# Optimization experiments

Measured on AMD Instinct MI355X. Metric: run time of the kernel, lower is better.

## Reference

```python
import jax, jax.numpy as jnp
import numpy as np

D_MODEL = 1024
N_HEADS = 16
D_HEAD = D_MODEL // N_HEADS
ROPE_THETA = 10000.0


def apply_rope(x, positions):
    # x: [b, h, s, d], positions: [s]
    half = x.shape[-1] // 2
    inv_freq = ROPE_THETA ** (-jnp.arange(half, dtype=x.dtype) * 2.0 / x.shape[-1])
    ang = positions.astype(x.dtype)[:, None] * inv_freq[None, :]  # [s, half]
    cos, sin = jnp.cos(ang), jnp.sin(ang)
    x1, x2 = x[..., 0::2], x[..., 1::2]  # rotate interleaved pairs (x_{2k}, x_{2k+1})
    out_even = x1 * cos - x2 * sin
    out_odd = x1 * sin + x2 * cos
    return jnp.stack([out_even, out_odd], axis=-1).reshape(x.shape)


def setup_inputs() -> dict:
    key = jax.random.key(0)
    k1, k2, k3 = jax.random.split(key, 3)
    b, s = 4, 2048
    x = jax.random.normal(k1, (b, s, D_MODEL), dtype=jnp.float32)
    w_qkv = jax.random.normal(k2, (3 * D_MODEL, D_MODEL), dtype=jnp.float32) * (D_MODEL ** -0.5)
    w_out = jax.random.normal(k3, (D_MODEL, D_MODEL), dtype=jnp.float32) * (D_MODEL ** -0.5)
    return {"x": x, "w_qkv": w_qkv, "w_out": w_out}


def reference(x, w_qkv, w_out):
    b, s, _ = x.shape
    qkv = jnp.einsum('bsd,ed->bse', x, w_qkv)  # fused QKV projection
    qkv = qkv.reshape(b, s, 3, N_HEADS, D_HEAD).transpose(2, 0, 3, 1, 4)  # [3, b, h, s, d]
    q, k, v = qkv[0], qkv[1], qkv[2]
    positions = jnp.arange(s)
    q = apply_rope(q, positions)
    k = apply_rope(k, positions)
    scale = 1.0 / np.sqrt(D_HEAD)
    scores = jnp.einsum('bhqd,bhkd->bhqk', q, k) * scale
    causal = jnp.tril(jnp.ones((s, s), dtype=bool))
    scores = jnp.where(causal, scores, jnp.finfo(scores.dtype).min)
    attn = jax.nn.softmax(scores, axis=-1)
    out = jnp.einsum('bhqk,bhkd->bhqd', attn, v)
    out = out.transpose(0, 2, 1, 3).reshape(b, s, D_MODEL)  # b h s d -> b s (h d)
    return jnp.einsum('bsd,ed->bse', out, w_out)
```

## Files before the change

### kernel.cpp

```cpp
#include <hip/hip_runtime.h>
#include <math.h>

#define D_MODEL 1024
#define NH      16
#define DH      64
#define S_LEN   2048
#define BATCH   4

typedef unsigned short u16;
typedef __attribute__((ext_vector_type(8))) short s8v;
typedef __attribute__((ext_vector_type(4))) float f4v;

#define MFMA(a, b, c) __builtin_amdgcn_mfma_f32_16x16x32_bf16((a), (b), (c), 0, 0, 0)

__device__ inline u16 f2bf(float f) {
  unsigned u = __float_as_uint(f);
  u += 0x7fffu + ((u >> 16) & 1u);
  return (u16)(u >> 16);
}
__device__ inline float bf2f(u16 h) {
  return __uint_as_float(((unsigned)h) << 16);
}
__device__ inline u16 f2bf_trunc(float f) {
  return (u16)(__float_as_uint(f) >> 16);
}
__device__ inline void split4(const float4 v, short4& h4, short4& l4) {
  u16 hx = f2bf(v.x), hy = f2bf(v.y), hz = f2bf(v.z), hw = f2bf(v.w);
  h4 = make_short4((short)hx, (short)hy, (short)hz, (short)hw);
  l4 = make_short4((short)f2bf_trunc(v.x - bf2f(hx)), (short)f2bf_trunc(v.y - bf2f(hy)),
                   (short)f2bf_trunc(v.z - bf2f(hz)), (short)f2bf_trunc(v.w - bf2f(hw)));
}

__global__ void rope_table_kernel(float* __restrict__ tab) {
  int i = blockIdx.x * 256 + threadIdx.x;
  if (i >= S_LEN * 32) return;
  int s = i >> 5;
  int p = i & 31;
  float invf = (float)pow(10000.0, -(double)p / 32.0);
  float ang = (float)s * invf;
  tab[i]         = cosf(ang);
  tab[65536 + i] = sinf(ang);
}

template <int MODE>
__global__ __launch_bounds__(256) void gemm_mfma(
    const float* __restrict__ A, const float* __restrict__ B,
    float* __restrict__ C,
    u16* __restrict__ qh, u16* __restrict__ ql,
    u16* __restrict__ kh, u16* __restrict__ kl,
    float* __restrict__ vw,
    const float* __restrict__ tab,
    int M, int N, int K)
{
  __shared__ short As[2][128][40];
  __shared__ short Bs[2][128][40];

  const int tid  = threadIdx.x;
  const int lane = tid & 63;
  const int wave = tid >> 6;
  const int wm = wave >> 1, wn = wave & 1;
  const int m0 = blockIdx.y * 128;
  const int n0 = blockIdx.x * 128;

  const int lr = lane & 15;
  const int lk = (lane >> 4) * 8;

  f4v acc[4][4] = {};

  float4 av[4], bv[4];
#pragma unroll
  for (int q = 0; q < 4; ++q) {
    int f = q * 256 + tid;
    int r = f >> 3, kk = (f & 7) * 4;
    av[q] = *(const float4*)&A[(size_t)(m0 + r) * K + kk];
    bv[q] = *(const float4*)&B[(size_t)(n0 + r) * K + kk];
  }

  for (int k0 = 0; k0 < K; k0 += 32) {
    __syncthreads();
#pragma unroll
    for (int q = 0; q < 4; ++q) {
      int f = q * 256 + tid;
      int r = f >> 3, kk = (f & 7) * 4;
      short4 h4, l4;
      split4(av[q], h4, l4);
      *(short4*)&As[0][r][kk] = h4;  *(short4*)&As[1][r][kk] = l4;
      split4(bv[q], h4, l4);
      *(short4*)&Bs[0][r][kk] = h4;  *(short4*)&Bs[1][r][kk] = l4;
    }
    __syncthreads();

    if (k0 + 32 < K) {
#pragma unroll
      for (int q = 0; q < 4; ++q) {
        int f = q * 256 + tid;
        int r = f >> 3, kk = (f & 7) * 4;
        av[q] = *(const float4*)&A[(size_t)(m0 + r) * K + k0 + 32 + kk];
        bv[q] = *(const float4*)&B[(size_t)(n0 + r) * K + k0 + 32 + kk];
      }
    }

    s8v ah[4], al[4], bh[4], bl[4];
#pragma unroll
    for (int x = 0; x < 4; ++x) {
      ah[x] = *(const s8v*)&As[0][wm * 64 + x * 16 + lr][lk];
      al[x] = *(const s8v*)&As[1][wm * 64 + x * 16 + lr][lk];
      bh[x] = *(const s8v*)&Bs[0][wn * 64 + x * 16 + lr][lk];
      bl[x] = *(const s8v*)&Bs[1][wn * 64 + x * 16 + lr][lk];
    }
#pragma unroll
    for (int mf = 0; mf < 4; ++mf)
#pragma unroll
      for (int nf = 0; nf < 4; ++nf) {
        acc[mf][nf] = MFMA(ah[mf], bh[nf], acc[mf][nf]);
        acc[mf][nf] = MFMA(al[mf], bh[nf], acc[mf][nf]);
        acc[mf][nf] = MFMA(ah[mf], bl[nf], acc[mf][nf]);
      }
  }

  if (MODE == 0) {
#pragma unroll
    for (int mf = 0; mf < 4; ++mf)
#pragma unroll
      for (int nf = 0; nf < 4; ++nf) {
        int c = n0 + wn * 64 + nf * 16 + lr;
#pragma unroll
        for (int i = 0; i < 4; ++i) {
          int m = m0 + wm * 64 + mf * 16 + (lane >> 4) * 4 + i;
          C[(size_t)m * N + c] = acc[mf][nf][i];
        }
      }
  } else {
#pragma unroll
    for (int nf = 0; nf < 4; ++nf) {
      int c = n0 + wn * 64 + nf * 16 + lr;
      int t = c >> 10;
      int h = (c & 1023) >> 6;
      int d = c & 63;
#pragma unroll
      for (int mf = 0; mf < 4; ++mf)
#pragma unroll
        for (int i = 0; i < 4; ++i) {
          int m = m0 + wm * 64 + mf * 16 + (lane >> 4) * 4 + i;
          int b = m >> 11, s = m & 2047;
          float v  = acc[mf][nf][i];
          float pv = __shfl_xor(v, 1);
          size_t off = ((size_t)(b * NH + h) * S_LEN + s) * DH + d;
          if (t == 2) {
            vw[off] = v;
          } else {
            int p = d >> 1;
            float co = tab[s * 32 + p], si = tab[65536 + s * 32 + p];
            float res = ((d & 1) == 0) ? (v * co - pv * si)
                                       : (pv * si + v * co);
            u16 hi = f2bf(res);
            u16 lo = f2bf_trunc(res - bf2f(hi));
            ((t == 0) ? qh : kh)[off] = hi;
            ((t == 0) ? ql : kl)[off] = lo;
          }
        }
    }
  }
}

__global__ __launch_bounds__(256) void vtrans_kernel(
    const float* __restrict__ vw, u16* __restrict__ vth, u16* __restrict__ vtl)
{
  __shared__ float T[64][65];
  const int tid = threadIdx.x;
  const int st = blockIdx.x, bh = blockIdx.y;
  const int s0 = st * 64;
#pragma unroll
  for (int it = 0; it < 4; ++it) {
    int f = it * 256 + tid;
    int r = f >> 4, c4 = (f & 15) * 4;
    float4 v = *(const float4*)&vw[((size_t)bh * S_LEN + s0 + r) * DH + c4];
    T[r][c4 + 0] = v.x; T[r][c4 + 1] = v.y; T[r][c4 + 2] = v.z; T[r][c4 + 3] = v.w;
  }
  __syncthreads();
#pragma unroll
  for (int it = 0; it < 16; ++it) {
    int f = it * 256 + tid;
    int d = f >> 6, sc = f & 63;
    float v = T[sc][d];
    u16 hi = f2bf(v);
    size_t off = ((size_t)bh * DH + d) * S_LEN + s0 + sc;
    vth[off] = hi;
    vtl[off] = f2bf_trunc(v - bf2f(hi));
  }
}

__global__ __launch_bounds__(256) void attn3_kernel(
    const u16* __restrict__ qhp, const u16* __restrict__ qlp,
    const u16* __restrict__ khp, const u16* __restrict__ klp,
    const u16* __restrict__ vthp, const u16* __restrict__ vtlp,
    float* __restrict__ ow)
{
  __shared__ u16 Kh[64][72], Kl[64][72];
  __shared__ u16 Vh[64][72], Vl[64][72];
  __shared__ u16 Ph[4][16][72], Pl[4][16][72];

  const int tid  = threadIdx.x;
  const int lane = tid & 63;
  const int w    = tid >> 6;
  const int bid = blockIdx.x;
  const int swz = (bid & 7) * 256 + (bid >> 3);
  const int bh  = swz >> 5;
  const int qt  = 31 - (swz & 31);
  const int q0  = qt * 64;

  const int lr = lane & 15;
  const int lk = (lane >> 4) * 8;
  const int rg = (lane >> 4) * 4;

  const size_t kvbase = (size_t)bh * S_LEN * DH;
  const size_t vtbase = (size_t)bh * DH * S_LEN;

  const int sr  = tid >> 2;
  const int sc0 = (tid & 3) * 16;

  const u16* qrow_h = qhp + kvbase + (size_t)(q0 + w * 16 + lr) * DH;
  const u16* qrow_l = qlp + kvbase + (size_t)(q0 + w * 16 + lr) * DH;
  s8v qfh[2], qfl[2];
#pragma unroll
  for (int c = 0; c < 2; ++c) {
    qfh[c] = *(const s8v*)(qrow_h + c * 32 + lk);
    qfl[c] = *(const s8v*)(qrow_l + c * 32 + lk);
  }

  float m_run[4] = {-3.0e38f, -3.0e38f, -3.0e38f, -3.0e38f};
  float l_run[4] = {0.f, 0.f, 0.f, 0.f};
  f4v o[4] = {};

  s8v rkh[2], rkl[2], rvh[2], rvl[2];
  {
    const size_t koff = kvbase + (size_t)sr * DH + sc0;
    const size_t voff = vtbase + (size_t)sr * S_LEN + 0 + sc0;
    rkh[0] = *(const s8v*)(khp + koff);   rkh[1] = *(const s8v*)(khp + koff + 8);
    rkl[0] = *(const s8v*)(klp + koff);   rkl[1] = *(const s8v*)(klp + koff + 8);
    rvh[0] = *(const s8v*)(vthp + voff);  rvh[1] = *(const s8v*)(vthp + voff + 8);
    rvl[0] = *(const s8v*)(vtlp + voff);  rvl[1] = *(const s8v*)(vtlp + voff + 8);
  }

  for (int kt = 0; kt <= qt; ++kt) {
    __syncthreads();
    *(s8v*)&Kh[sr][sc0] = rkh[0];  *(s8v*)&Kh[sr][sc0 + 8] = rkh[1];
    *(s8v*)&Kl[sr][sc0] = rkl[0];  *(s8v*)&Kl[sr][sc0 + 8] = rkl[1];
    *(s8v*)&Vh[sr][sc0] = rvh[0];  *(s8v*)&Vh[sr][sc0 + 8] = rvh[1];
    *(s8v*)&Vl[sr][sc0] = rvl[0];  *(s8v*)&Vl[sr][sc0 + 8] = rvl[1];
    __syncthreads();

    if (kt < qt) {
      const int kn = (kt + 1) * 64;
      const size_t koff = kvbase + (size_t)(kn + sr) * DH + sc0;
      const size_t voff = vtbase + (size_t)sr * S_LEN + kn + sc0;
      rkh[0] = *(const s8v*)(khp + koff);   rkh[1] = *(const s8v*)(khp + koff + 8);
      rkl[0] = *(const s8v*)(klp + koff);   rkl[1] = *(const s8v*)(klp + koff + 8);
      rvh[0] = *(const s8v*)(vthp + voff);  rvh[1] = *(const s8v*)(vthp + voff + 8);
      rvl[0] = *(const s8v*)(vtlp + voff);  rvl[1] = *(const s8v*)(vtlp + voff + 8);
    }

    f4v sf[4] = {};
#pragma unroll
    for (int f = 0; f < 4; ++f)
#pragma unroll
      for (int c = 0; c < 2; ++c) {
        s8v kbh = *(const s8v*)&Kh[f * 16 + lr][c * 32 + lk];
        s8v kbl = *(const s8v*)&Kl[f * 16 + lr][c * 32 + lk];
        sf[f] = MFMA(qfh[c], kbh, sf[f]);
        sf[f] = MFMA(qfl[c], kbh, sf[f]);
        sf[f] = MFMA(qfh[c], kbl, sf[f]);
      }

    const bool diag = (kt == qt);
    float p[4][4];
    float sc[4][4];
#pragma unroll
    for (int f = 0; f < 4; ++f)
#pragma unroll
      for (int i = 0; i < 4; ++i) {
        float v = sf[f][i] * 0.125f;
        if (diag) {
          int col = f * 16 + lr;
          int row = w * 16 + rg + i;
          if (col > row) v = -3.0e38f;
        }
        sc[f][i] = v;
      }
#pragma unroll
    for (int i = 0; i < 4; ++i) {
      float mx = fmaxf(fmaxf(sc[0][i], sc[1][i]), fmaxf(sc[2][i], sc[3][i]));
#pragma unroll
      for (int off = 1; off < 16; off <<= 1) mx = fmaxf(mx, __shfl_xor(mx, off));
      float mnew  = fmaxf(m_run[i], mx);
      float alpha = __expf(m_run[i] - mnew);
      float rs = 0.f;
#pragma unroll
      for (int f = 0; f < 4; ++f) { p[f][i] = __expf(sc[f][i] - mnew); rs += p[f][i]; }
#pragma unroll
      for (int off = 1; off < 16; off <<= 1) rs += __shfl_xor(rs, off);
      l_run[i] = l_run[i] * alpha + rs;
      m_run[i] = mnew;
#pragma unroll
      for (int f2 = 0; f2 < 4; ++f2) o[f2][i] *= alpha;
    }

#pragma unroll
    for (int f = 0; f < 4; ++f)
#pragma unroll
      for (int i = 0; i < 4; ++i) {
        u16 hi = f2bf(p[f][i]);
        Ph[w][rg + i][f * 16 + lr] = hi;
        Pl[w][rg + i][f * 16 + lr] = f2bf_trunc(p[f][i] - bf2f(hi));
      }

#pragma unroll
    for (int c = 0; c < 2; ++c) {
      s8v pah = *(const s8v*)&Ph[w][lr][c * 32 + lk];
      s8v pal = *(const s8v*)&Pl[w][lr][c * 32 + lk];
#pragma unroll
      for (int f2 = 0; f2 < 4; ++f2) {
        s8v vbh = *(const s8v*)&Vh[f2 * 16 + lr][c * 32 + lk];
        s8v vbl = *(const s8v*)&Vl[f2 * 16 + lr][c * 32 + lk];
        o[f2] = MFMA(pah, vbh, o[f2]);
        o[f2] = MFMA(pal, vbh, o[f2]);
        o[f2] = MFMA(pah, vbl, o[f2]);
      }
    }
  }

  const int b = bh >> 4, h = bh & 15;
#pragma unroll
  for (int i = 0; i < 4; ++i) {
    int s = q0 + w * 16 + rg + i;
    float inv = 1.0f / l_run[i];
#pragma unroll
    for (int f2 = 0; f2 < 4; ++f2) {
      int d = f2 * 16 + lr;
      ow[((size_t)(b * S_LEN + s)) * D_MODEL + h * DH + d] = o[f2][i] * inv;
    }
  }
}

extern "C" void kernel_launch(void* const* d_in, const int* in_sizes, int n_in,
                              void* d_out, int out_size, void* d_ws, size_t ws_size,
                              hipStream_t stream) {
  const float* x     = (const float*)d_in[0];
  const float* w_qkv = (const float*)d_in[1];
  const float* w_out = (const float*)d_in[2];
  float* out = (float*)d_out;

  const size_t NQ = (size_t)BATCH * NH * S_LEN * DH;
  float* ws    = (float*)d_ws;
  float* tab   = ws;
  float* vw_ow = ws + 131072;
  u16*   us    = (u16*)(vw_ow + NQ);
  u16* qh  = us;            u16* ql  = qh + NQ;
  u16* kh  = ql + NQ;       u16* kl  = kh + NQ;
  u16* vth = kl + NQ;       u16* vtl = vth + NQ;

  const int M = BATCH * S_LEN;

  rope_table_kernel<<<(S_LEN * 32 + 255) / 256, 256, 0, stream>>>(tab);

  gemm_mfma<1><<<dim3(3 * D_MODEL / 128, M / 128), 256, 0, stream>>>(
      x, w_qkv, nullptr, qh, ql, kh, kl, vw_ow, tab, M, 3 * D_MODEL, D_MODEL);

  vtrans_kernel<<<dim3(S_LEN / 64, BATCH * NH), 256, 0, stream>>>(vw_ow, vth, vtl);

  attn3_kernel<<<dim3(S_LEN / 64 * BATCH * NH), 256, 0, stream>>>(
      qh, ql, kh, kl, vth, vtl, vw_ow);

  gemm_mfma<0><<<dim3(D_MODEL / 128, M / 128), 256, 0, stream>>>(
      vw_ow, w_out, out, nullptr, nullptr, nullptr, nullptr, nullptr, tab,
      M, D_MODEL, D_MODEL);
}
```

Measured before the change: 627.3 us.

## Pre-split GEMM operands to bf16 hi/lo and drop split precision for PV

Adds a split kernel that converts x, w_qkv and w_out to bf16 hi/lo pairs once, so the GEMMs load pre-split bf16 tiles instead of converting fp32 in every block. The attention kernel now uses a single bf16 for V and P in the PV product, removing two of three MFMAs plus the V-low loads and stores, and it writes its output as hi/lo bf16 for the output projection. This removes repeated conversion work and cuts PV compute and memory traffic, at the cost of extra split passes, more workspace, and lower PV accuracy.

```diff
diff --git a/kernel.cpp b/kernel.cpp
--- a/kernel.cpp
+++ b/kernel.cpp
@@ -42,9 +42,21 @@
   tab[65536 + i] = sinf(ang);
 }
 
+__global__ __launch_bounds__(256) void split_kernel(
+    const float* __restrict__ src, u16* __restrict__ dh, u16* __restrict__ dl, int n4) {
+  int i = blockIdx.x * 256 + threadIdx.x;
+  if (i >= n4) return;
+  float4 v = reinterpret_cast<const float4*>(src)[i];
+  short4 h4, l4;
+  split4(v, h4, l4);
+  reinterpret_cast<short4*>(dh)[i] = h4;
+  reinterpret_cast<short4*>(dl)[i] = l4;
+}
+
 template <int MODE>
-__global__ __launch_bounds__(256) void gemm_mfma(
-    const float* __restrict__ A, const float* __restrict__ B,
+__global__ __launch_bounds__(256) void gemm2(
+    const u16* __restrict__ Ah, const u16* __restrict__ Al,
+    const u16* __restrict__ Bh, const u16* __restrict__ Bl,
     float* __restrict__ C,
     u16* __restrict__ qh, u16* __restrict__ ql,
     u16* __restrict__ kh, u16* __restrict__ kl,
@@ -52,8 +64,8 @@
     const float* __restrict__ tab,
     int M, int N, int K)
 {
-  __shared__ short As[2][128][40];
-  __shared__ short Bs[2][128][40];
+  __shared__ u16 As[2][128][40];
+  __shared__ u16 Bs[2][128][40];
 
   const int tid  = threadIdx.x;
   const int lane = tid & 63;
@@ -65,39 +77,36 @@
   const int lr = lane & 15;
   const int lk = (lane >> 4) * 8;
 
+  const int srow = tid >> 1;
+  const int skc  = (tid & 1) * 16;
+
   f4v acc[4][4] = {};
 
-  float4 av[4], bv[4];
-#pragma unroll
-  for (int q = 0; q < 4; ++q) {
-    int f = q * 256 + tid;
-    int r = f >> 3, kk = (f & 7) * 4;
-    av[q] = *(const float4*)&A[(size_t)(m0 + r) * K + kk];
-    bv[q] = *(const float4*)&B[(size_t)(n0 + r) * K + kk];
+  s8v ra[2][2], rb[2][2];
+  {
+    const size_t ab = (size_t)(m0 + srow) * K + skc;
+    const size_t bb = (size_t)(n0 + srow) * K + skc;
+    ra[0][0] = *(const s8v*)(Ah + ab);  ra[0][1] = *(const s8v*)(Ah + ab + 8);
+    ra[1][0] = *(const s8v*)(Al + ab);  ra[1][1] = *(const s8v*)(Al + ab + 8);
+    rb[0][0] = *(const s8v*)(Bh + bb);  rb[0][1] = *(const s8v*)(Bh + bb + 8);
+    rb[1][0] = *(const s8v*)(Bl + bb);  rb[1][1] = *(const s8v*)(Bl + bb + 8);
   }
 
   for (int k0 = 0; k0 < K; k0 += 32) {
     __syncthreads();
-#pragma unroll
-    for (int q = 0; q < 4; ++q) {
-      int f = q * 256 + tid;
-      int r = f >> 3, kk = (f & 7) * 4;
-      short4 h4, l4;
-      split4(av[q], h4, l4);
-      *(short4*)&As[0][r][kk] = h4;  *(short4*)&As[1][r][kk] = l4;
-      split4(bv[q], h4, l4);
-      *(short4*)&Bs[0][r][kk] = h4;  *(short4*)&Bs[1][r][kk] = l4;
-    }
+    *(s8v*)&As[0][srow][skc] = ra[0][0];  *(s8v*)&As[0][srow][skc + 8] = ra[0][1];
+    *(s8v*)&As[1][srow][skc] = ra[1][0];  *(s8v*)&As[1][srow][skc + 8] = ra[1][1];
+    *(s8v*)&Bs[0][srow][skc] = rb[0][0];  *(s8v*)&Bs[0][srow][skc + 8] = rb[0][1];
+    *(s8v*)&Bs[1][srow][skc] = rb[1][0];  *(s8v*)&Bs[1][srow][skc + 8] = rb[1][1];
     __syncthreads();
 
     if (k0 + 32 < K) {
-#pragma unroll
-      for (int q = 0; q < 4; ++q) {
-        int f = q * 256 + tid;
-        int r = f >> 3, kk = (f & 7) * 4;
-        av[q] = *(const float4*)&A[(size_t)(m0 + r) * K + k0 + 32 + kk];
-        bv[q] = *(const float4*)&B[(size_t)(n0 + r) * K + k0 + 32 + kk];
-      }
+      const size_t ab = (size_t)(m0 + srow) * K + k0 + 32 + skc;
+      const size_t bb = (size_t)(n0 + srow) * K + k0 + 32 + skc;
+      ra[0][0] = *(const s8v*)(Ah + ab);  ra[0][1] = *(const s8v*)(Ah + ab + 8);
+      ra[1][0] = *(const s8v*)(Al + ab);  ra[1][1] = *(const s8v*)(Al + ab + 8);
+      rb[0][0] = *(const s8v*)(Bh + bb);  rb[0][1] = *(const s8v*)(Bh + bb + 8);
+      rb[1][0] = *(const s8v*)(Bl + bb);  rb[1][1] = *(const s8v*)(Bl + bb + 8);
     }
 
     s8v ah[4], al[4], bh[4], bl[4];
@@ -164,7 +173,7 @@
 }
 
 __global__ __launch_bounds__(256) void vtrans_kernel(
-    const float* __restrict__ vw, u16* __restrict__ vth, u16* __restrict__ vtl)
+    const float* __restrict__ vw, u16* __restrict__ vth)
 {
   __shared__ float T[64][65];
   const int tid = threadIdx.x;
@@ -182,23 +191,19 @@
   for (int it = 0; it < 16; ++it) {
     int f = it * 256 + tid;
     int d = f >> 6, sc = f & 63;
-    float v = T[sc][d];
-    u16 hi = f2bf(v);
-    size_t off = ((size_t)bh * DH + d) * S_LEN + s0 + sc;
-    vth[off] = hi;
-    vtl[off] = f2bf_trunc(v - bf2f(hi));
-  }
-}
-
-__global__ __launch_bounds__(256) void attn3_kernel(
+    vth[((size_t)bh * DH + d) * S_LEN + s0 + sc] = f2bf(T[sc][d]);
+  }
+}
+
+__global__ __launch_bounds__(256) void attn4_kernel(
     const u16* __restrict__ qhp, const u16* __restrict__ qlp,
     const u16* __restrict__ khp, const u16* __restrict__ klp,
-    const u16* __restrict__ vthp, const u16* __restrict__ vtlp,
-    float* __restrict__ ow)
+    const u16* __restrict__ vthp,
+    u16* __restrict__ ohp, u16* __restrict__ olp)
 {
   __shared__ u16 Kh[64][72], Kl[64][72];
-  __shared__ u16 Vh[64][72], Vl[64][72];
-  __shared__ u16 Ph[4][16][72], Pl[4][16][72];
+  __shared__ u16 Vh[64][72];
+  __shared__ u16 Ph[4][16][72];
 
   const int tid  = threadIdx.x;
   const int lane = tid & 63;
@@ -232,14 +237,13 @@
   float l_run[4] = {0.f, 0.f, 0.f, 0.f};
   f4v o[4] = {};
 
-  s8v rkh[2], rkl[2], rvh[2], rvl[2];
+  s8v rkh[2], rkl[2], rvh[2];
   {
     const size_t koff = kvbase + (size_t)sr * DH + sc0;
-    const size_t voff = vtbase + (size_t)sr * S_LEN + 0 + sc0;
+    const size_t voff = vtbase + (size_t)sr * S_LEN + sc0;
     rkh[0] = *(const s8v*)(khp + koff);   rkh[1] = *(const s8v*)(khp + koff + 8);
     rkl[0] = *(const s8v*)(klp + koff);   rkl[1] = *(const s8v*)(klp + koff + 8);
     rvh[0] = *(const s8v*)(vthp + voff);  rvh[1] = *(const s8v*)(vthp + voff + 8);
-    rvl[0] = *(const s8v*)(vtlp + voff);  rvl[1] = *(const s8v*)(vtlp + voff + 8);
   }
 
   for (int kt = 0; kt <= qt; ++kt) {
@@ -247,7 +251,6 @@
     *(s8v*)&Kh[sr][sc0] = rkh[0];  *(s8v*)&Kh[sr][sc0 + 8] = rkh[1];
     *(s8v*)&Kl[sr][sc0] = rkl[0];  *(s8v*)&Kl[sr][sc0 + 8] = rkl[1];
     *(s8v*)&Vh[sr][sc0] = rvh[0];  *(s8v*)&Vh[sr][sc0 + 8] = rvh[1];
-    *(s8v*)&Vl[sr][sc0] = rvl[0];  *(s8v*)&Vl[sr][sc0 + 8] = rvl[1];
     __syncthreads();
 
     if (kt < qt) {
@@ -257,7 +260,6 @@
       rkh[0] = *(const s8v*)(khp + koff);   rkh[1] = *(const s8v*)(khp + koff + 8);
       rkl[0] = *(const s8v*)(klp + koff);   rkl[1] = *(const s8v*)(klp + koff + 8);
       rvh[0] = *(const s8v*)(vthp + voff);  rvh[1] = *(const s8v*)(vthp + voff + 8);
-      rvl[0] = *(const s8v*)(vtlp + voff);  rvl[1] = *(const s8v*)(vtlp + voff + 8);
     }
 
     f4v sf[4] = {};
@@ -308,23 +310,16 @@
 #pragma unroll
     for (int f = 0; f < 4; ++f)
 #pragma unroll
-      for (int i = 0; i < 4; ++i) {
-        u16 hi = f2bf(p[f][i]);
-        Ph[w][rg + i][f * 16 + lr] = hi;
-        Pl[w][rg + i][f * 16 + lr] = f2bf_trunc(p[f][i] - bf2f(hi));
-      }
+      for (int i = 0; i < 4; ++i)
+        Ph[w][rg + i][f * 16 + lr] = f2bf(p[f][i]);
 
 #pragma unroll
     for (int c = 0; c < 2; ++c) {
       s8v pah = *(const s8v*)&Ph[w][lr][c * 32 + lk];
-      s8v pal = *(const s8v*)&Pl[w][lr][c * 32 + lk];
 #pragma unroll
       for (int f2 = 0; f2 < 4; ++f2) {
         s8v vbh = *(const s8v*)&Vh[f2 * 16 + lr][c * 32 + lk];
-        s8v vbl = *(const s8v*)&Vl[f2 * 16 + lr][c * 32 + lk];
         o[f2] = MFMA(pah, vbh, o[f2]);
-        o[f2] = MFMA(pal, vbh, o[f2]);
-        o[f2] = MFMA(pah, vbl, o[f2]);
       }
     }
   }
@@ -337,7 +332,11 @@
 #pragma unroll
     for (int f2 = 0; f2 < 4; ++f2) {
       int d = f2 * 16 + lr;
-      ow[((size_t)(b * S_LEN + s)) * D_MODEL + h * DH + d] = o[f2][i] * inv;
+      float val = o[f2][i] * inv;
+      size_t off = ((size_t)(b * S_LEN + s)) * D_MODEL + h * DH + d;
+      u16 hi = f2bf(val);
+      ohp[off] = hi;
+      olp[off] = f2bf_trunc(val - bf2f(hi));
     }
   }
 }
@@ -351,27 +350,44 @@
   float* out = (float*)d_out;
 
   const size_t NQ = (size_t)BATCH * NH * S_LEN * DH;
-  float* ws    = (float*)d_ws;
-  float* tab   = ws;
-  float* vw_ow = ws + 131072;
-  u16*   us    = (u16*)(vw_ow + NQ);
-  u16* qh  = us;            u16* ql  = qh + NQ;
-  u16* kh  = ql + NQ;       u16* kl  = kh + NQ;
-  u16* vth = kl + NQ;       u16* vtl = vth + NQ;
+  const size_t NWQ = (size_t)3 * D_MODEL * D_MODEL;
+  const size_t NWO = (size_t)D_MODEL * D_MODEL;
+
+  float* ws  = (float*)d_ws;
+  float* tab = ws;
+  float* vw  = ws + 131072;
+  u16* u   = (u16*)(vw + NQ);
+  u16* xh  = u;  u += NQ;
+  u16* xl  = u;  u += NQ;
+  u16* wqh = u;  u += NWQ;
+  u16* wql = u;  u += NWQ;
+  u16* woh = u;  u += NWO;
+  u16* wol = u;  u += NWO;
+  u16* qh  = u;  u += NQ;
+  u16* ql  = u;  u += NQ;
+  u16* kh  = u;  u += NQ;
+  u16* kl  = u;  u += NQ;
+  u16* vth = u;  u += NQ;
 
   const int M = BATCH * S_LEN;
 
   rope_table_kernel<<<(S_LEN * 32 + 255) / 256, 256, 0, stream>>>(tab);
 
-  gemm_mfma<1><<<dim3(3 * D_MODEL / 128, M / 128), 256, 0, stream>>>(
-      x, w_qkv, nullptr, qh, ql, kh, kl, vw_ow, tab, M, 3 * D_MODEL, D_MODEL);
-
-  vtrans_kernel<<<dim3(S_LEN / 64, BATCH * NH), 256, 0, stream>>>(vw_ow, vth, vtl);
-
-  attn3_kernel<<<dim3(S_LEN / 64 * BATCH * NH), 256, 0, stream>>>(
-      qh, ql, kh, kl, vth, vtl, vw_ow);
-
-  gemm_mfma<0><<<dim3(D_MODEL / 128, M / 128), 256, 0, stream>>>(
-      vw_ow, w_out, out, nullptr, nullptr, nullptr, nullptr, nullptr, tab,
+  split_kernel<<<(int)(NQ / 4 + 255) / 256, 256, 0, stream>>>(x, xh, xl, (int)(NQ / 4));
+  split_kernel<<<(int)(NWQ / 4 + 255) / 256, 256, 0, stream>>>(w_qkv, wqh, wql, (int)(NWQ / 4));
+  split_kernel<<<(int)(NWO / 4 + 255) / 256, 256, 0, stream>>>(w_out, woh, wol, (int)(NWO / 4));
+
+  gemm2<1><<<dim3(3 * D_MODEL / 128, M / 128), 256, 0, stream>>>(
+      xh, xl, wqh, wql, nullptr, qh, ql, kh, kl, vw, tab, M, 3 * D_MODEL, D_MODEL);
+
+  vtrans_kernel<<<dim3(S_LEN / 64, BATCH * NH), 256, 0, stream>>>(vw, vth);
+
+  u16* oh = xh;
+  u16* ol = xl;
+  attn4_kernel<<<dim3(S_LEN / 64 * BATCH * NH), 256, 0, stream>>>(
+      qh, ql, kh, kl, vth, oh, ol);
+
+  gemm2<0><<<dim3(D_MODEL / 128, M / 128), 256, 0, stream>>>(
+      oh, ol, woh, wol, out, nullptr, nullptr, nullptr, nullptr, nullptr, tab,
       M, D_MODEL, D_MODEL);
 }
```

Measured after the change: 548.6 us. 12.6% less time.
